# Optimization experiments

Measured on AMD Instinct MI355X. Metric: run time of the kernel, lower is better.

Reference implementation:

```python
import jax, jax.numpy as jnp
import numpy as np

WD, WH, WW = 6, 6, 6
NUM_HEADS = 8
EPS = 1e-5


def setup_inputs() -> dict:
    key = jax.random.key(0)
    ks = jax.random.split(key, 4)
    B, C, D, H, W = 1, 128, 48, 48, 48
    return {
        "q_map": jax.random.normal(ks[0], (B, C, D, H, W), dtype=jnp.float32),
        "k_map": jax.random.normal(ks[1], (B, C, D, H, W), dtype=jnp.float32),
        "v_map": jax.random.normal(ks[2], (B, C, D, H, W), dtype=jnp.float32),
        "gamma_q": jnp.ones((C,), jnp.float32),
        "beta_q": jnp.zeros((C,), jnp.float32),
        "gamma_kv": jnp.ones((C,), jnp.float32),
        "beta_kv": jnp.zeros((C,), jnp.float32),
        "proj_w": jax.random.normal(ks[3], (C, C), dtype=jnp.float32) * (1.0 / np.sqrt(C)),
        "proj_b": jnp.zeros((C,), jnp.float32),
    }


def _layernorm(x, g, b):
    m = jnp.mean(x, axis=-1, keepdims=True)
    v = jnp.mean(jnp.square(x - m), axis=-1, keepdims=True)
    return (x - m) * jax.lax.rsqrt(v + EPS) * g + b


def _window_partition(x):
    # x: (B, D, H, W, C) -> windows: (B*nD*nH*nW, wd*wh*ww, C)
    B, D, H, W, C = x.shape
    pd, ph, pw = (WD - D % WD) % WD, (WH - H % WH) % WH, (WW - W % WW) % WW
    if pd or ph or pw:
        x = jnp.pad(x, ((0, 0), (0, pd), (0, ph), (0, pw), (0, 0)))
    Dp, Hp, Wp = D + pd, H + ph, W + pw
    x = x.reshape(B, Dp // WD, WD, Hp // WH, WH, Wp // WW, WW, C)
    x = jnp.transpose(x, (0, 1, 3, 5, 2, 4, 6, 7))
    return x.reshape(-1, WD * WH * WW, C), (D, H, W, Dp, Hp, Wp)


def _window_reverse(windows, meta):
    D, H, W, Dp, Hp, Wp = meta
    C = windows.shape[-1]
    nD, nH, nW = Dp // WD, Hp // WH, Wp // WW
    B = windows.shape[0] // (nD * nH * nW)
    x = windows.reshape(B, nD, nH, nW, WD, WH, WW, C)
    x = jnp.transpose(x, (0, 1, 4, 2, 5, 3, 6, 7)).reshape(B, Dp, Hp, Wp, C)
    return x[:, :D, :H, :W, :]


def reference(q_map, k_map, v_map, gamma_q, beta_q, gamma_kv, beta_kv, proj_w, proj_b):
    # (B, C, D, H, W) -> (B, D, H, W, C)
    q_map = jnp.transpose(q_map, (0, 2, 3, 4, 1))
    k_map = jnp.transpose(k_map, (0, 2, 3, 4, 1))
    v_map = jnp.transpose(v_map, (0, 2, 3, 4, 1))

    q, meta = _window_partition(q_map)
    k, _ = _window_partition(k_map)
    v, _ = _window_partition(v_map)

    q = _layernorm(q, gamma_q, beta_q)
    k = _layernorm(k, gamma_kv, beta_kv)
    v = _layernorm(v, gamma_kv, beta_kv)

    Bw, Nq, C = q.shape
    dh = C // NUM_HEADS
    q = q.reshape(Bw, Nq, NUM_HEADS, dh)
    k = k.reshape(Bw, -1, NUM_HEADS, dh)
    v = v.reshape(Bw, -1, NUM_HEADS, dh)

    scale = 1.0 / np.sqrt(dh).astype(np.float32)
    scores = jnp.einsum("bqhd,bkhd->bhqk", q, k) * scale  # (Bw, h, Nq, Nk)
    attn = jax.nn.softmax(scores, axis=-1)
    out = jnp.einsum("bhqk,bkhd->bqhd", attn, v).reshape(Bw, Nq, C)

    out = out @ proj_w.T + proj_b
    out = _window_reverse(out, meta)
    return jnp.transpose(out, (0, 4, 1, 2, 3))  # (B, C, D, H, W)
```

## Files before the change

### kernel.cpp

```cpp
#include <hip/hip_runtime.h>
#include <hip/hip_bf16.h>

typedef short s16x8 __attribute__((ext_vector_type(8)));
typedef float f32x2 __attribute__((ext_vector_type(2)));
typedef float f32x4 __attribute__((ext_vector_type(4)));
typedef float f32x16 __attribute__((ext_vector_type(16)));
typedef unsigned int u32;
typedef unsigned short u16;
typedef u32 u32x4v __attribute__((ext_vector_type(4)));

#define TOK 216
#define T1 448
#define T2 896
#define SP 110592
#define BUF0 0
#define VOFF 57344
#define WOFF 122880
#define GBOFF 155648
#define LDS_OLD 157696
#define LDS_NEW 155648
#define TENB 28311552ull
#define WSNEED (3ull*TENB + 32768ull)
#define QSCALE 0.360673760f

__device__ __forceinline__ u32 pack2(float a, float b) {
  u16 lo = __builtin_bit_cast(u16, __float2bfloat16(a));
  u16 hi = __builtin_bit_cast(u16, __float2bfloat16(b));
  return (u32)lo | ((u32)hi << 16);
}
__device__ __forceinline__ int swz(int row, int inner) {
  return inner ^ ((row & 7) << 4);
}
__device__ __forceinline__ int swzk(int row, int inner) {
  return inner ^ ((row & 15) << 4);
}
__device__ __forceinline__ void gload16(const void* g, void* l) {
  __builtin_amdgcn_global_load_lds(
      (const __attribute__((address_space(1))) void*)g,
      (__attribute__((address_space(3))) void*)l, 16, 0, 0);
}

__device__ __forceinline__ void ln_stats(const f32x2* xv, float& mA, float& rA,
                                         float& mB, float& rB) {
  float sA = 0.f, s2A = 0.f, sB = 0.f, s2B = 0.f;
#pragma unroll
  for (int c = 0; c < 32; ++c) {
    sA += xv[c].x; s2A += xv[c].x * xv[c].x;
    sB += xv[c].y; s2B += xv[c].y * xv[c].y;
  }
  sA += __shfl_xor(sA, 1); s2A += __shfl_xor(s2A, 1);
  sB += __shfl_xor(sB, 1); s2B += __shfl_xor(s2B, 1);
  sA += __shfl_xor(sA, 2); s2A += __shfl_xor(s2A, 2);
  sB += __shfl_xor(sB, 2); s2B += __shfl_xor(s2B, 2);
  mA = sA * (1.0f / 128.0f);
  rA = rsqrtf(s2A * (1.0f / 128.0f) - mA * mA + 1e-5f);
  mB = sB * (1.0f / 128.0f);
  rB = rsqrtf(s2B * (1.0f / 128.0f) - mB * mB + 1e-5f);
}

template<bool MASK>
__device__ __forceinline__ void attn_stepN(const char* smem, int h, int kt,
                                           s16x8 qfh, int lane,
                                           f32x16& acc, float& lsum) {
  const int half = lane >> 5;
  const int krow = kt * 32 + (lane & 31);
  s16x8 kf = *(const s16x8*)(smem + BUF0 + krow * 256 +
                             swzk(krow, h * 32 + half * 16));
  f32x16 st = __builtin_amdgcn_mfma_f32_32x32x16_bf16(kf, qfh, (f32x16){}, 0, 0, 0);
  const int vrow = h * 16 + (lane & 15);
  s16x8 vf0 = *(const s16x8*)(smem + VOFF + vrow * 512 +
                              swz(vrow, kt * 64 + half * 16));
  s16x8 vf1 = *(const s16x8*)(smem + VOFF + vrow * 512 +
                              swz(vrow, kt * 64 + 32 + half * 16));
  const int NR = MASK ? 12 : 16;
  u32 A[8];
  float ts0 = 0.f, ts1 = 0.f;
#pragma unroll
  for (int i = 0; i < 8; ++i) {
    float p0 = (2 * i < NR) ? __builtin_amdgcn_exp2f(st[2 * i]) : 0.f;
    float p1 = (2 * i + 1 < NR) ? __builtin_amdgcn_exp2f(st[2 * i + 1]) : 0.f;
    if (i & 1) ts1 += p0 + p1; else ts0 += p0 + p1;
    A[i] = pack2(p0, p1);
  }
  lsum += ts0 + ts1;
  s16x8 pf0 = __builtin_bit_cast(s16x8, (u32x4v){A[0], A[1], A[2], A[3]});
  s16x8 pf1 = __builtin_bit_cast(s16x8, (u32x4v){A[4], A[5], A[6], A[7]});
  acc = __builtin_amdgcn_mfma_f32_32x32x16_bf16(vf0, pf0, acc, 0, 0, 0);
  acc = __builtin_amdgcn_mfma_f32_32x32x16_bf16(vf1, pf1, acc, 0, 0, 0);
}

template<bool MASK>
__device__ __forceinline__ void attn_stepF(const char* smem, int h, int kt,
                                           s16x8 qfh, int lane,
                                           f32x16& acc, float& lsum) {
  const int half = lane >> 5;
  const int krow = kt * 32 + (lane & 31);
  s16x8 kf = *(const s16x8*)(smem + BUF0 + krow * 256 +
                             swz(krow, h * 32 + half * 16));
  f32x16 st = __builtin_amdgcn_mfma_f32_32x32x16_bf16(kf, qfh, (f32x16){}, 0, 0, 0);
  const int vrow = h * 16 + (lane & 15);
  s16x8 vf0 = *(const s16x8*)(smem + VOFF + vrow * 512 +
                              swz(vrow, kt * 64 + half * 16));
  s16x8 vf1 = *(const s16x8*)(smem + VOFF + vrow * 512 +
                              swz(vrow, kt * 64 + 32 + half * 16));
  const int NR = MASK ? 12 : 16;
  u32 A[8];
  float ts0 = 0.f, ts1 = 0.f;
#pragma unroll
  for (int i = 0; i < 8; ++i) {
    float p0 = (2 * i < NR) ? __builtin_amdgcn_exp2f(st[2 * i]) : 0.f;
    float p1 = (2 * i + 1 < NR) ? __builtin_amdgcn_exp2f(st[2 * i + 1]) : 0.f;
    if (i & 1) ts1 += p0 + p1; else ts0 += p0 + p1;
    A[i] = pack2(p0, p1);
  }
  lsum += ts0 + ts1;
  s16x8 pf0 = __builtin_bit_cast(s16x8, (u32x4v){A[0], A[1], A[2], A[3]});
  s16x8 pf1 = __builtin_bit_cast(s16x8, (u32x4v){A[4], A[5], A[6], A[7]});
  acc = __builtin_amdgcn_mfma_f32_32x32x16_bf16(vf0, pf0, acc, 0, 0, 0);
  acc = __builtin_amdgcn_mfma_f32_32x32x16_bf16(vf1, pf1, acc, 0, 0, 0);
}

extern "C" __global__ __launch_bounds__(256)
void lnpre_kernel(const float* __restrict__ qm, const float* __restrict__ km,
                  const float* __restrict__ vm,
                  const float* __restrict__ gq, const float* __restrict__ bq,
                  const float* __restrict__ gkv, const float* __restrict__ bkv,
                  const float* __restrict__ pw,
                  u16* __restrict__ qn, u16* __restrict__ kn,
                  u16* __restrict__ vn, u16* __restrict__ wbf) {
  const int tid = threadIdx.x;
  const int bid = blockIdx.x;
  if (bid >= 2304) {
#pragma unroll
    for (int k = 0; k < 32; ++k) {
      int idx = tid + 256 * k;
      f32x2 w2 = *(const f32x2*)(pw + idx * 2);
      ((u32*)wbf)[idx] = pack2(w2.x, w2.y);
    }
    return;
  }
  __shared__ float lf[6144];
  __shared__ float gb[512];
  const int d = bid / 48, h = bid - d * 48;
  const int dh = d * 2304 + h * 48;
  if (tid < 128) {
    gb[tid] = gq[tid]; gb[128 + tid] = bq[tid];
    gb[256 + tid] = gkv[tid]; gb[384 + tid] = bkv[tid];
  }
  const int w = tid >> 2, q = tid & 3;
#pragma unroll 1
  for (int t = 0; t < 3; ++t) {
    const float* src = t == 0 ? qm : (t == 1 ? km : vm);
    u16* dst = t == 0 ? qn : (t == 1 ? kn : vn);
    const float* g = (t == 0) ? gb : gb + 256;
    const float* b = (t == 0) ? gb + 128 : gb + 384;
    const float scale = (t == 0) ? QSCALE : 1.0f;
#pragma unroll
    for (int k = 0; k < 6; ++k) {
      int j = tid + 256 * k;
      int ch = j / 12, wq = j - ch * 12;
      *(f32x4*)(lf + ch * 48 + wq * 4) =
          *(const f32x4*)(src + (long)ch * SP + dh + wq * 4);
    }
    __syncthreads();
    if (tid < 192) {
      float s = 0.f, s2 = 0.f;
#pragma unroll
      for (int c = 0; c < 32; ++c) {
        float x = lf[(q + 4 * c) * 48 + w];
        s += x; s2 += x * x;
      }
      s += __shfl_xor(s, 1); s2 += __shfl_xor(s2, 1);
      s += __shfl_xor(s, 2); s2 += __shfl_xor(s2, 2);
      float m = s * (1.f / 128.f);
      float r = rsqrtf(s2 * (1.f / 128.f) - m * m + 1e-5f);
      u32x4v* op = (u32x4v*)(dst + (long)(dh + w) * 128 + 32 * q);
#pragma unroll
      for (int v4 = 0; v4 < 4; ++v4) {
        u32x4v pk;
#pragma unroll
        for (int e = 0; e < 4; ++e) {
          int ch = 32 * q + v4 * 8 + 2 * e;
          float y0 = ((lf[ch * 48 + w] - m) * r * g[ch] + b[ch]) * scale;
          float y1 = ((lf[(ch + 1) * 48 + w] - m) * r * g[ch + 1] + b[ch + 1]) * scale;
          pk[e] = pack2(y0, y1);
        }
        op[v4] = pk;
      }
    }
    __syncthreads();
  }
}

extern "C" __global__ __launch_bounds__(T2, 1)
void attn2_kernel(const u16* __restrict__ qn, const u16* __restrict__ kn,
                  const u16* __restrict__ vn, const u16* __restrict__ wbf,
                  const float* __restrict__ pb, float* __restrict__ out) {
  extern __shared__ __align__(16) char smem[];
  const int tid = threadIdx.x;
  const int lane = tid & 63;
  const int wv = tid >> 6;
  const int wq = wv % 7;
  const int hb = (wv / 7) * 4;
  const int bid = blockIdx.x;
  const int wid = ((bid & 7) << 6) | (bid >> 3);
  const int wd = wid >> 6, wh = (wid >> 3) & 7, ww = wid & 7;
  const int wd6 = wd * 6, wh6 = wh * 6, ww6 = ww * 6;
  const int boff = wd6 * 2304 + wh6 * 48 + ww6;

  for (int uu = wv; uu < 140; uu += 14) {
    const u16* s; char* d;
    if (uu < 54) {
      int u = uu, row = 4 * u + (lane >> 4);
      int tq = row / 6;
      int g = (wd6 + tq / 6) * 2304 + (wh6 + tq % 6) * 48 + ww6 + row % 6;
      s = qn + g * 128 + (((lane & 15) ^ (row & 15)) << 3);
      d = smem + BUF0 + u * 1024;
    } else if (uu < 108) {
      int u = uu - 54, row = 4 * u + (lane >> 4);
      int tq = row / 6;
      int g = (wd6 + tq / 6) * 2304 + (wh6 + tq % 6) * 48 + ww6 + row % 6;
      s = vn + g * 128 + ((lane & 15) << 3);
      d = smem + VOFF + u * 1024;
    } else {
      int u = uu - 108, row = 4 * u + (lane >> 4);
      s = wbf + row * 128 + (((lane & 15) ^ (row & 15)) << 3);
      d = smem + WOFF + u * 1024;
    }
    gload16(s, d);
  }
  __syncthreads();

  s16x8 qf[4];
  {
    int row = wq * 32 + (lane & 31);
    int ib = (lane >> 5) * 16;
#pragma unroll
    for (int j = 0; j < 4; ++j)
      qf[j] = *(const s16x8*)(smem + BUF0 + row * 256 +
                              swzk(row, (hb + j) * 32 + ib));
  }
  __syncthreads();

  for (int uu = wv; uu < 54; uu += 14) {
    int row = 4 * uu + (lane >> 4);
    int tq = row / 6;
    int g = (wd6 + tq / 6) * 2304 + (wh6 + tq % 6) * 48 + ww6 + row % 6;
    gload16(kn + g * 128 + (((lane & 15) ^ (row & 15)) << 3),
            smem + BUF0 + uu * 1024);
  }
  u32 tr[16];
#pragma unroll
  for (int k = 0; k < 8; ++k) {
    int u = tid + 896 * k;
    if (u < 6912) {
      int t = (u >> 6) * 2, c2 = u & 63;
      tr[2 * k]     = *(const u32*)(smem + VOFF + t * 256 + c2 * 4);
      tr[2 * k + 1] = *(const u32*)(smem + VOFF + t * 256 + 256 + c2 * 4);
    }
  }
  __syncthreads();

#pragma unroll
  for (int k = 0; k < 8; ++k) {
    int u = tid + 896 * k;
    if (u < 6912) {
      int t = (u >> 6) * 2, c2 = u & 63;
      int st = (t & ~12) | ((t & 4) << 1) | ((t & 8) >> 1);
      int c = 2 * c2;
      u32 w0 = (tr[2 * k] & 0xFFFFu) | (tr[2 * k + 1] << 16);
      u32 w1 = (tr[2 * k] >> 16) | (tr[2 * k + 1] & 0xFFFF0000u);
      *(u32*)(smem + VOFF + c * 512 + ((st * 2) ^ ((c & 7) << 4))) = w0;
      *(u32*)(smem + VOFF + (c + 1) * 512 + ((st * 2) ^ (((c + 1) & 7) << 4))) = w1;
    }
  }
  if (tid < 128) {
    int x = (tid & 7) << 4;
    *(u32*)(smem + VOFF + tid * 512 + (424 ^ x)) = 0;
    *(u32*)(smem + VOFF + tid * 512 + (428 ^ x)) = 0;
    *(u32*)(smem + VOFF + tid * 512 + (440 ^ x)) = 0;
    *(u32*)(smem + VOFF + tid * 512 + (444 ^ x)) = 0;
  }
  __syncthreads();

  u32 oPk[4][4];
#pragma unroll
  for (int hp = 0; hp < 2; ++hp) {
    const int h0 = hb + 2 * hp, h1 = h0 + 1;
    f32x16 a0 = {}, a1 = {};
    float l0 = 0.f, l1 = 0.f;
#pragma unroll 2
    for (int kt = 0; kt < 6; ++kt) {
      attn_stepN<false>(smem, h0, kt, qf[2 * hp], lane, a0, l0);
      attn_stepN<false>(smem, h1, kt, qf[2 * hp + 1], lane, a1, l1);
    }
    attn_stepN<true>(smem, h0, 6, qf[2 * hp], lane, a0, l0);
    attn_stepN<true>(smem, h1, 6, qf[2 * hp + 1], lane, a1, l1);
    l0 += __shfl_xor(l0, 32);
    l1 += __shfl_xor(l1, 32);
    float i0 = 1.0f / l0, i1 = 1.0f / l1;
#pragma unroll
    for (int r = 0; r < 4; ++r) {
      oPk[2 * hp][r]     = pack2(a0[2 * r] * i0, a0[2 * r + 1] * i0);
      oPk[2 * hp + 1][r] = pack2(a1[2 * r] * i1, a1[2 * r + 1] * i1);
    }
  }
  __syncthreads();

  {
    const int tok = wq * 32 + (lane & 31);
    const int half = lane >> 5;
#pragma unroll
    for (int j = 0; j < 4; ++j) {
      int chb = (hb + j) * 32 + half * 8;
      *(u32*)(smem + BUF0 + tok * 256 + swzk(tok, chb))      = oPk[j][0];
      *(u32*)(smem + BUF0 + tok * 256 + swzk(tok, chb + 4))  = oPk[j][1];
      *(u32*)(smem + BUF0 + tok * 256 + swzk(tok, chb + 16)) = oPk[j][2];
      *(u32*)(smem + BUF0 + tok * 256 + swzk(tok, chb + 20)) = oPk[j][3];
    }
  }
  __syncthreads();

  {
    int tok = wv * 16 + (lane & 15);
    s16x8 bfr[4];
#pragma unroll
    for (int kk = 0; kk < 4; ++kk)
      bfr[kk] = *(const s16x8*)(smem + BUF0 + tok * 256 +
                                swzk(tok, kk * 64 + (lane >> 4) * 16));
    bool tokValid = tok < TOK;
    int tdd = tok / 36, trr = tok - tdd * 36;
    int thh = trr / 6, tww = trr - thh * 6;
    int pos = boff + tdd * 2304 + thh * 48 + tww;
#pragma unroll 1
    for (int jt = 0; jt < 8; ++jt) {
      f32x4 acc = {};
#pragma unroll
      for (int kk = 0; kk < 4; ++kk) {
        int rw = jt * 16 + (lane & 15);
        s16x8 af = *(const s16x8*)(smem + WOFF + rw * 256 +
                                   swzk(rw, kk * 64 + (lane >> 4) * 16));
        acc = __builtin_amdgcn_mfma_f32_16x16x32_bf16(af, bfr[kk], acc, 0, 0, 0);
      }
      f32x4 pbv = *(const f32x4*)(pb + jt * 16 + (lane >> 4) * 4);
      if (tokValid) {
#pragma unroll
        for (int r = 0; r < 4; ++r) {
          int j = jt * 16 + (lane >> 4) * 4 + r;
          out[j * SP + pos] = acc[r] + pbv[r];
        }
      }
    }
  }
}

extern "C" __global__ __launch_bounds__(T1, 2)
void ca3d_kernel(const float* __restrict__ qm, const float* __restrict__ km,
                 const float* __restrict__ vm,
                 const float* __restrict__ gq, const float* __restrict__ bq,
                 const float* __restrict__ gkv, const float* __restrict__ bkv,
                 const float* __restrict__ pw, const float* __restrict__ pb,
                 float* __restrict__ out) {
  extern __shared__ __align__(16) char smem[];
  const int tid = threadIdx.x;
  const int lane = tid & 63;
  const int wv = tid >> 6;
  const int bid = blockIdx.x;
  const int wid = ((bid & 7) << 6) | (bid >> 3);
  const int wd = wid >> 6, wh = (wid >> 3) & 7, ww = wid & 7;
  const int boff = wd * 6 * 2304 + wh * 6 * 48 + ww * 6;

  for (int i = tid * 16; i < VOFF + 65536; i += T1 * 16)
    *(f32x4*)(smem + i) = (f32x4){};
  if (tid < 128) {
    ((float*)(smem + GBOFF))[tid] = gq[tid];
    ((float*)(smem + GBOFF + 512))[tid] = bq[tid];
    ((float*)(smem + GBOFF + 1024))[tid] = gkv[tid];
    ((float*)(smem + GBOFF + 1536))[tid] = bkv[tid];
  }
  const bool lnAct = tid < 432;
  const int tp = tid >> 2;
  const int cbase = (tid & 3) * 32;
  const int tA = tp * 2, tB = tA + 1;
  int td = tA / 36, tr_ = tA - td * 36;
  int th_ = tr_ / 6, tw_ = tr_ - th_ * 6;
  const int gpos = boff + td * 2304 + th_ * 48 + tw_;
  const int vposA = (tA & ~0xC) | ((tA & 4) << 1) | ((tA & 8) >> 1);

  f32x2 qv[32], kv[32], vv[32];
  if (lnAct) {
#pragma unroll
    for (int c = 0; c < 32; ++c)
      qv[c] = *(const f32x2*)(qm + gpos + (cbase + c) * SP);
#pragma unroll
    for (int c = 0; c < 32; ++c)
      kv[c] = *(const f32x2*)(km + gpos + (cbase + c) * SP);
  }
  __syncthreads();
  const float* gql = (const float*)(smem + GBOFF);
  const float* bql = (const float*)(smem + GBOFF + 512);
  const float* gkl = (const float*)(smem + GBOFF + 1024);
  const float* bkl = (const float*)(smem + GBOFF + 1536);
  if (lnAct) {
    float mA, rA, mB, rB;
    ln_stats(qv, mA, rA, mB, rB);
#pragma unroll
    for (int c = 0; c < 32; c += 2) {
      int cc = cbase + c;
      float g0 = gql[cc], g1 = gql[cc + 1], b0 = bql[cc], b1 = bql[cc + 1];
      *(u32*)(smem + BUF0 + tA * 256 + swz(tA, cc * 2)) =
          pack2(((qv[c].x - mA) * rA * g0 + b0) * QSCALE,
                ((qv[c + 1].x - mA) * rA * g1 + b1) * QSCALE);
      *(u32*)(smem + BUF0 + tB * 256 + swz(tB, cc * 2)) =
          pack2(((qv[c].y - mB) * rB * g0 + b0) * QSCALE,
                ((qv[c + 1].y - mB) * rB * g1 + b1) * QSCALE);
    }
#pragma unroll
    for (int c = 0; c < 32; ++c)
      vv[c] = *(const f32x2*)(vm + gpos + (cbase + c) * SP);
  }
  __syncthreads();
  s16x8 qf[8];
  {
    int row = wv * 32 + (lane & 31);
    int ib = (lane >> 5) * 16;
#pragma unroll
    for (int h = 0; h < 8; ++h)
      qf[h] = *(const s16x8*)(smem + BUF0 + row * 256 + swz(row, h * 32 + ib));
  }
  __syncthreads();
  if (lnAct) {
    {
      float mA, rA, mB, rB;
      ln_stats(kv, mA, rA, mB, rB);
#pragma unroll
      for (int c = 0; c < 32; c += 2) {
        int cc = cbase + c;
        float g0 = gkl[cc], g1 = gkl[cc + 1], b0 = bkl[cc], b1 = bkl[cc + 1];
        *(u32*)(smem + BUF0 + tA * 256 + swz(tA, cc * 2)) =
            pack2((kv[c].x - mA) * rA * g0 + b0,
                  (kv[c + 1].x - mA) * rA * g1 + b1);
        *(u32*)(smem + BUF0 + tB * 256 + swz(tB, cc * 2)) =
            pack2((kv[c].y - mB) * rB * g0 + b0,
                  (kv[c + 1].y - mB) * rB * g1 + b1);
      }
    }
    {
      float mA, rA, mB, rB;
      ln_stats(vv, mA, rA, mB, rB);
#pragma unroll
      for (int c = 0; c < 32; ++c) {
        int cc = cbase + c;
        float g0 = gkl[cc], b0 = bkl[cc];
        *(u32*)(smem + VOFF + cc * 512 + swz(cc, vposA * 2)) =
            pack2((vv[c].x - mA) * rA * g0 + b0,
                  (vv[c].y - mB) * rB * g0 + b0);
      }
    }
  }
  for (int i = tid; i < 8192; i += T1) {
    int j = i >> 6, c2 = i & 63;
    f32x2 w2 = *(const f32x2*)(pw + j * 128 + c2 * 2);
    *(u32*)(smem + WOFF + j * 256 + swz(j, c2 * 4)) = pack2(w2.x, w2.y);
  }
  __syncthreads();
  u32 oPk[8][4];
#pragma unroll
  for (int hp = 0; hp < 4; ++hp) {
    const int h0 = hp * 2, h1 = h0 + 1;
    f32x16 a0 = {}, a1 = {};
    float l0 = 0.f, l1 = 0.f;
#pragma unroll 1
    for (int kt = 0; kt < 6; ++kt) {
      attn_stepF<false>(smem, h0, kt, qf[h0], lane, a0, l0);
      attn_stepF<false>(smem, h1, kt, qf[h1], lane, a1, l1);
    }
    attn_stepF<true>(smem, h0, 6, qf[h0], lane, a0, l0);
    attn_stepF<true>(smem, h1, 6, qf[h1], lane, a1, l1);
    l0 += __shfl_xor(l0, 32);
    l1 += __shfl_xor(l1, 32);
    float i0 = 1.0f / l0, i1 = 1.0f / l1;
#pragma unroll
    for (int r = 0; r < 4; ++r) {
      oPk[h0][r] = pack2(a0[2 * r] * i0, a0[2 * r + 1] * i0);
      oPk[h1][r] = pack2(a1[2 * r] * i1, a1[2 * r + 1] * i1);
    }
  }
  __syncthreads();
  {
    const int tok = wv * 32 + (lane & 31);
    const int half = lane >> 5;
#pragma unroll
    for (int h = 0; h < 8; ++h) {
      int chb = h * 32 + half * 8;
      *(u32*)(smem + BUF0 + tok * 256 + swz(tok, chb))      = oPk[h][0];
      *(u32*)(smem + BUF0 + tok * 256 + swz(tok, chb + 4))  = oPk[h][1];
      *(u32*)(smem + BUF0 + tok * 256 + swz(tok, chb + 16)) = oPk[h][2];
      *(u32*)(smem + BUF0 + tok * 256 + swz(tok, chb + 20)) = oPk[h][3];
    }
  }
  __syncthreads();
#pragma unroll 1
  for (int ti = 0; ti < 2; ++ti) {
    int tt = wv * 2 + ti;
    int tok = tt * 16 + (lane & 15);
    s16x8 bfr[4];
#pragma unroll
    for (int kk = 0; kk < 4; ++kk)
      bfr[kk] = *(const s16x8*)(smem + BUF0 + tok * 256 +
                                swz(tok, kk * 64 + (lane >> 4) * 16));
    bool tokValid = tok < TOK;
    int tdd = tok / 36, trr = tok - tdd * 36;
    int thh = trr / 6, tww = trr - thh * 6;
    int pos = boff + tdd * 2304 + thh * 48 + tww;
#pragma unroll 1
    for (int jt = 0; jt < 8; ++jt) {
      f32x4 acc = {};
#pragma unroll
      for (int kk = 0; kk < 4; ++kk) {
        int rw = jt * 16 + (lane & 15);
        s16x8 af = *(const s16x8*)(smem + WOFF + rw * 256 +
                                   swz(rw, kk * 64 + (lane >> 4) * 16));
        acc = __builtin_amdgcn_mfma_f32_16x16x32_bf16(af, bfr[kk], acc, 0, 0, 0);
      }
      f32x4 pbv = *(const f32x4*)(pb + jt * 16 + (lane >> 4) * 4);
      if (tokValid) {
#pragma unroll
        for (int r = 0; r < 4; ++r) {
          int j = jt * 16 + (lane >> 4) * 4 + r;
          out[j * SP + pos] = acc[r] + pbv[r];
        }
      }
    }
  }
}

extern "C" void kernel_launch(void* const* d_in, const int* in_sizes, int n_in,
                              void* d_out, int out_size, void* d_ws, size_t ws_size,
                              hipStream_t stream) {
  const float* qm  = (const float*)d_in[0];
  const float* km  = (const float*)d_in[1];
  const float* vm  = (const float*)d_in[2];
  const float* gq  = (const float*)d_in[3];
  const float* bq  = (const float*)d_in[4];
  const float* gkv = (const float*)d_in[5];
  const float* bkv = (const float*)d_in[6];
  const float* pw  = (const float*)d_in[7];
  const float* pb  = (const float*)d_in[8];
  if (ws_size >= WSNEED) {
    u16* qn  = (u16*)d_ws;
    u16* kn  = (u16*)((char*)d_ws + TENB);
    u16* vn  = (u16*)((char*)d_ws + 2 * TENB);
    u16* wbf = (u16*)((char*)d_ws + 3 * TENB);
    hipLaunchKernelGGL(lnpre_kernel, dim3(2305), dim3(256), 0, stream,
                       qm, km, vm, gq, bq, gkv, bkv, pw, qn, kn, vn, wbf);
    hipLaunchKernelGGL(attn2_kernel, dim3(512), dim3(T2), LDS_NEW, stream,
                       qn, kn, vn, wbf, pb, (float*)d_out);
  } else {
    hipLaunchKernelGGL(ca3d_kernel, dim3(512), dim3(T1), LDS_OLD, stream,
                       qm, km, vm, gq, bq, gkv, bkv, pw, pb, (float*)d_out);
  }
}
```

Before: 149.9 us.

## Split attention into per-head-group kernel and separate projection kernel

Replaces the single 896-thread attention+projection kernel, which used about 152KB of LDS and ran one block per CU, with two kernels. The first handles half the heads per block, uses 60KB of static LDS to allow several blocks per CU, and writes the attention output back into the q buffer in place. The second does the output projection over rows of 48 tokens so the stores to the output are coalesced. The cost is an extra launch and a bf16 round trip of the attention output through global memory.

```diff
diff --git a/kernel.cpp b/kernel.cpp
--- a/kernel.cpp
+++ b/kernel.cpp
@@ -11,14 +11,13 @@
 
 #define TOK 216
 #define T1 448
-#define T2 896
 #define SP 110592
 #define BUF0 0
 #define VOFF 57344
 #define WOFF 122880
 #define GBOFF 155648
 #define LDS_OLD 157696
-#define LDS_NEW 155648
+#define VHOFF 28672
 #define TENB 28311552ull
 #define WSNEED (3ull*TENB + 32768ull)
 #define QSCALE 0.360673760f
@@ -30,9 +29,6 @@
 }
 __device__ __forceinline__ int swz(int row, int inner) {
   return inner ^ ((row & 7) << 4);
-}
-__device__ __forceinline__ int swzk(int row, int inner) {
-  return inner ^ ((row & 15) << 4);
 }
 __device__ __forceinline__ void gload16(const void* g, void* l) {
   __builtin_amdgcn_global_load_lds(
@@ -59,19 +55,19 @@
 }
 
 template<bool MASK>
-__device__ __forceinline__ void attn_stepN(const char* smem, int h, int kt,
+__device__ __forceinline__ void attn_stepH(const char* smem, int jloc, int kt,
                                            s16x8 qfh, int lane,
                                            f32x16& acc, float& lsum) {
   const int half = lane >> 5;
   const int krow = kt * 32 + (lane & 31);
-  s16x8 kf = *(const s16x8*)(smem + BUF0 + krow * 256 +
-                             swzk(krow, h * 32 + half * 16));
+  s16x8 kf = *(const s16x8*)(smem + krow * 128 +
+                             ((jloc * 32 + half * 16) ^ ((krow & 7) << 4)));
   f32x16 st = __builtin_amdgcn_mfma_f32_32x32x16_bf16(kf, qfh, (f32x16){}, 0, 0, 0);
-  const int vrow = h * 16 + (lane & 15);
-  s16x8 vf0 = *(const s16x8*)(smem + VOFF + vrow * 512 +
-                              swz(vrow, kt * 64 + half * 16));
-  s16x8 vf1 = *(const s16x8*)(smem + VOFF + vrow * 512 +
-                              swz(vrow, kt * 64 + 32 + half * 16));
+  const int vrow = jloc * 16 + (lane & 15);
+  s16x8 vf0 = *(const s16x8*)(smem + VHOFF + vrow * 512 +
+                              ((kt * 64 + half * 16) ^ ((vrow & 7) << 4)));
+  s16x8 vf1 = *(const s16x8*)(smem + VHOFF + vrow * 512 +
+                              ((kt * 64 + 32 + half * 16) ^ ((vrow & 7) << 4)));
   const int NR = MASK ? 12 : 16;
   u32 A[8];
   float ts0 = 0.f, ts1 = 0.f;
@@ -192,163 +188,167 @@
   }
 }
 
-extern "C" __global__ __launch_bounds__(T2, 1)
-void attn2_kernel(const u16* __restrict__ qn, const u16* __restrict__ kn,
-                  const u16* __restrict__ vn, const u16* __restrict__ wbf,
-                  const float* __restrict__ pb, float* __restrict__ out) {
-  extern __shared__ __align__(16) char smem[];
-  const int tid = threadIdx.x;
-  const int lane = tid & 63;
-  const int wv = tid >> 6;
-  const int wq = wv % 7;
-  const int hb = (wv / 7) * 4;
+extern "C" __global__ __launch_bounds__(448, 4)
+void attnh_kernel(u16* __restrict__ qn, const u16* __restrict__ kn,
+                  const u16* __restrict__ vn) {
+  __shared__ __align__(16) char smem[61440];
+  const int tid = threadIdx.x, lane = tid & 63, wv = tid >> 6;
+  const int half = lane >> 5;
   const int bid = blockIdx.x;
-  const int wid = ((bid & 7) << 6) | (bid >> 3);
-  const int wd = wid >> 6, wh = (wid >> 3) & 7, ww = wid & 7;
-  const int wd6 = wd * 6, wh6 = wh * 6, ww6 = ww * 6;
-  const int boff = wd6 * 2304 + wh6 * 48 + ww6;
-
-  for (int uu = wv; uu < 140; uu += 14) {
-    const u16* s; char* d;
-    if (uu < 54) {
-      int u = uu, row = 4 * u + (lane >> 4);
-      int tq = row / 6;
-      int g = (wd6 + tq / 6) * 2304 + (wh6 + tq % 6) * 48 + ww6 + row % 6;
-      s = qn + g * 128 + (((lane & 15) ^ (row & 15)) << 3);
-      d = smem + BUF0 + u * 1024;
-    } else if (uu < 108) {
-      int u = uu - 54, row = 4 * u + (lane >> 4);
-      int tq = row / 6;
-      int g = (wd6 + tq / 6) * 2304 + (wh6 + tq % 6) * 48 + ww6 + row % 6;
-      s = vn + g * 128 + ((lane & 15) << 3);
-      d = smem + VOFF + u * 1024;
-    } else {
-      int u = uu - 108, row = 4 * u + (lane >> 4);
-      s = wbf + row * 128 + (((lane & 15) ^ (row & 15)) << 3);
-      d = smem + WOFF + u * 1024;
-    }
-    gload16(s, d);
-  }
-  __syncthreads();
-
-  s16x8 qf[4];
-  {
-    int row = wq * 32 + (lane & 31);
-    int ib = (lane >> 5) * 16;
-#pragma unroll
-    for (int j = 0; j < 4; ++j)
-      qf[j] = *(const s16x8*)(smem + BUF0 + row * 256 +
-                              swzk(row, (hb + j) * 32 + ib));
-  }
-  __syncthreads();
-
-  for (int uu = wv; uu < 54; uu += 14) {
-    int row = 4 * uu + (lane >> 4);
+  const int wid = bid >> 1, hg = bid & 1;
+  const int wd6 = (wid >> 6) * 6, wh6 = ((wid >> 3) & 7) * 6, ww6 = (wid & 7) * 6;
+
+  for (int uu = wv; uu < 27; uu += 7) {
+    int row = 8 * uu + (lane >> 3);
     int tq = row / 6;
     int g = (wd6 + tq / 6) * 2304 + (wh6 + tq % 6) * 48 + ww6 + row % 6;
-    gload16(kn + g * 128 + (((lane & 15) ^ (row & 15)) << 3),
-            smem + BUF0 + uu * 1024);
-  }
+    gload16(kn + g * 128 + hg * 64 + (((lane & 7) ^ (row & 7)) << 3),
+            smem + uu * 1024);
+  }
+  for (int uu = wv; uu < 27; uu += 7) {
+    int row = 8 * uu + (lane >> 3);
+    int tq = row / 6;
+    int g = (wd6 + tq / 6) * 2304 + (wh6 + tq % 6) * 48 + ww6 + row % 6;
+    gload16(vn + g * 128 + hg * 64 + ((lane & 7) << 3),
+            smem + VHOFF + uu * 1024);
+  }
+  int qrow = wv * 32 + (lane & 31);
+  if (qrow > 215) qrow = 215;
+  int qtq = qrow / 6;
+  int qg = (wd6 + qtq / 6) * 2304 + (wh6 + qtq % 6) * 48 + ww6 + qrow % 6;
+  s16x8 qf[4];
+#pragma unroll
+  for (int j = 0; j < 4; ++j)
+    qf[j] = *(const s16x8*)(qn + qg * 128 + (hg * 4 + j) * 16 + half * 8);
+  __syncthreads();
+
   u32 tr[16];
 #pragma unroll
   for (int k = 0; k < 8; ++k) {
-    int u = tid + 896 * k;
-    if (u < 6912) {
-      int t = (u >> 6) * 2, c2 = u & 63;
-      tr[2 * k]     = *(const u32*)(smem + VOFF + t * 256 + c2 * 4);
-      tr[2 * k + 1] = *(const u32*)(smem + VOFF + t * 256 + 256 + c2 * 4);
-    }
-  }
-  __syncthreads();
-
+    int u = tid + 448 * k;
+    if (u < 3456) {
+      int t = (u >> 5) * 2, c2 = u & 31;
+      tr[2 * k]     = *(const u32*)(smem + VHOFF + t * 128 + c2 * 4);
+      tr[2 * k + 1] = *(const u32*)(smem + VHOFF + t * 128 + 128 + c2 * 4);
+    }
+  }
+  __syncthreads();
 #pragma unroll
   for (int k = 0; k < 8; ++k) {
-    int u = tid + 896 * k;
-    if (u < 6912) {
-      int t = (u >> 6) * 2, c2 = u & 63;
+    int u = tid + 448 * k;
+    if (u < 3456) {
+      int t = (u >> 5) * 2, c2 = u & 31;
       int st = (t & ~12) | ((t & 4) << 1) | ((t & 8) >> 1);
       int c = 2 * c2;
       u32 w0 = (tr[2 * k] & 0xFFFFu) | (tr[2 * k + 1] << 16);
       u32 w1 = (tr[2 * k] >> 16) | (tr[2 * k + 1] & 0xFFFF0000u);
-      *(u32*)(smem + VOFF + c * 512 + ((st * 2) ^ ((c & 7) << 4))) = w0;
-      *(u32*)(smem + VOFF + (c + 1) * 512 + ((st * 2) ^ (((c + 1) & 7) << 4))) = w1;
-    }
-  }
-  if (tid < 128) {
+      *(u32*)(smem + VHOFF + c * 512 + ((st * 2) ^ ((c & 7) << 4))) = w0;
+      *(u32*)(smem + VHOFF + (c + 1) * 512 + ((st * 2) ^ (((c + 1) & 7) << 4))) = w1;
+    }
+  }
+  if (tid < 64) {
     int x = (tid & 7) << 4;
-    *(u32*)(smem + VOFF + tid * 512 + (424 ^ x)) = 0;
-    *(u32*)(smem + VOFF + tid * 512 + (428 ^ x)) = 0;
-    *(u32*)(smem + VOFF + tid * 512 + (440 ^ x)) = 0;
-    *(u32*)(smem + VOFF + tid * 512 + (444 ^ x)) = 0;
+    *(u32*)(smem + VHOFF + tid * 512 + (424 ^ x)) = 0;
+    *(u32*)(smem + VHOFF + tid * 512 + (428 ^ x)) = 0;
+    *(u32*)(smem + VHOFF + tid * 512 + (440 ^ x)) = 0;
+    *(u32*)(smem + VHOFF + tid * 512 + (444 ^ x)) = 0;
   }
   __syncthreads();
 
   u32 oPk[4][4];
 #pragma unroll
   for (int hp = 0; hp < 2; ++hp) {
-    const int h0 = hb + 2 * hp, h1 = h0 + 1;
+    const int j0 = 2 * hp, j1 = j0 + 1;
     f32x16 a0 = {}, a1 = {};
     float l0 = 0.f, l1 = 0.f;
 #pragma unroll 2
     for (int kt = 0; kt < 6; ++kt) {
-      attn_stepN<false>(smem, h0, kt, qf[2 * hp], lane, a0, l0);
-      attn_stepN<false>(smem, h1, kt, qf[2 * hp + 1], lane, a1, l1);
-    }
-    attn_stepN<true>(smem, h0, 6, qf[2 * hp], lane, a0, l0);
-    attn_stepN<true>(smem, h1, 6, qf[2 * hp + 1], lane, a1, l1);
+      attn_stepH<false>(smem, j0, kt, qf[j0], lane, a0, l0);
+      attn_stepH<false>(smem, j1, kt, qf[j1], lane, a1, l1);
+    }
+    attn_stepH<true>(smem, j0, 6, qf[j0], lane, a0, l0);
+    attn_stepH<true>(smem, j1, 6, qf[j1], lane, a1, l1);
     l0 += __shfl_xor(l0, 32);
     l1 += __shfl_xor(l1, 32);
     float i0 = 1.0f / l0, i1 = 1.0f / l1;
 #pragma unroll
     for (int r = 0; r < 4; ++r) {
-      oPk[2 * hp][r]     = pack2(a0[2 * r] * i0, a0[2 * r + 1] * i0);
-      oPk[2 * hp + 1][r] = pack2(a1[2 * r] * i1, a1[2 * r + 1] * i1);
+      oPk[j0][r] = pack2(a0[2 * r] * i0, a0[2 * r + 1] * i0);
+      oPk[j1][r] = pack2(a1[2 * r] * i1, a1[2 * r + 1] * i1);
     }
   }
   __syncthreads();
 
   {
-    const int tok = wq * 32 + (lane & 31);
-    const int half = lane >> 5;
+    const int tok = wv * 32 + (lane & 31);
 #pragma unroll
     for (int j = 0; j < 4; ++j) {
-      int chb = (hb + j) * 32 + half * 8;
-      *(u32*)(smem + BUF0 + tok * 256 + swzk(tok, chb))      = oPk[j][0];
-      *(u32*)(smem + BUF0 + tok * 256 + swzk(tok, chb + 4))  = oPk[j][1];
-      *(u32*)(smem + BUF0 + tok * 256 + swzk(tok, chb + 16)) = oPk[j][2];
-      *(u32*)(smem + BUF0 + tok * 256 + swzk(tok, chb + 20)) = oPk[j][3];
-    }
-  }
-  __syncthreads();
-
-  {
-    int tok = wv * 16 + (lane & 15);
-    s16x8 bfr[4];
+      int chb = j * 32 + half * 8;
+      *(u32*)(smem + tok * 128 + ((chb)      ^ ((tok & 7) << 4))) = oPk[j][0];
+      *(u32*)(smem + tok * 128 + ((chb + 4)  ^ ((tok & 7) << 4))) = oPk[j][1];
+      *(u32*)(smem + tok * 128 + ((chb + 16) ^ ((tok & 7) << 4))) = oPk[j][2];
+      *(u32*)(smem + tok * 128 + ((chb + 20) ^ ((tok & 7) << 4))) = oPk[j][3];
+    }
+  }
+  __syncthreads();
+
+#pragma unroll
+  for (int it = 0; it < 4; ++it) {
+    int i = tid + 448 * it;
+    int row = i >> 3;
+    if (row < 216) {
+      int chunk = i & 7;
+      f32x4 v = *(const f32x4*)(smem + row * 128 +
+                                ((chunk * 16) ^ ((row & 7) << 4)));
+      int tq = row / 6;
+      int g = (wd6 + tq / 6) * 2304 + (wh6 + tq % 6) * 48 + ww6 + row % 6;
+      *(f32x4*)(qn + g * 128 + hg * 64 + chunk * 8) = v;
+    }
+  }
+}
+
+extern "C" __global__ __launch_bounds__(256, 3)
+void proj_kernel(const u16* __restrict__ on, const u16* __restrict__ wbf,
+                 const float* __restrict__ pb, float* __restrict__ out) {
+  __shared__ __align__(16) char smem[45056];
+  const int tid = threadIdx.x, lane = tid & 63, wv = tid >> 6;
+  const int bid = blockIdx.x;
+  const int dh = (bid / 48) * 2304 + (bid % 48) * 48;
+  for (int uu = wv; uu < 32; uu += 4) {
+    int row = 4 * uu + (lane >> 4);
+    gload16(wbf + row * 128 + (((lane & 15) ^ (row & 15)) << 3),
+            smem + uu * 1024);
+  }
+  for (int uu = wv; uu < 12; uu += 4) {
+    int row = 4 * uu + (lane >> 4);
+    gload16(on + (long)(dh + row) * 128 + (((lane & 15) ^ (row & 15)) << 3),
+            smem + 32768 + uu * 1024);
+  }
+  __syncthreads();
+#pragma unroll
+  for (int jj = 0; jj < 2; ++jj) {
+    int jt = wv * 2 + jj;
+    int rw = jt * 16 + (lane & 15);
+    s16x8 af[4];
 #pragma unroll
     for (int kk = 0; kk < 4; ++kk)
-      bfr[kk] = *(const s16x8*)(smem + BUF0 + tok * 256 +
-                                swzk(tok, kk * 64 + (lane >> 4) * 16));
-    bool tokValid = tok < TOK;
-    int tdd = tok / 36, trr = tok - tdd * 36;
-    int thh = trr / 6, tww = trr - thh * 6;
-    int pos = boff + tdd * 2304 + thh * 48 + tww;
-#pragma unroll 1
-    for (int jt = 0; jt < 8; ++jt) {
+      af[kk] = *(const s16x8*)(smem + rw * 256 +
+                               ((kk * 64 + (lane >> 4) * 16) ^ ((rw & 15) << 4)));
+    f32x4 pbv = *(const f32x4*)(pb + jt * 16 + (lane >> 4) * 4);
+#pragma unroll
+    for (int t = 0; t < 3; ++t) {
+      int tok = t * 16 + (lane & 15);
       f32x4 acc = {};
 #pragma unroll
       for (int kk = 0; kk < 4; ++kk) {
-        int rw = jt * 16 + (lane & 15);
-        s16x8 af = *(const s16x8*)(smem + WOFF + rw * 256 +
-                                   swzk(rw, kk * 64 + (lane >> 4) * 16));
-        acc = __builtin_amdgcn_mfma_f32_16x16x32_bf16(af, bfr[kk], acc, 0, 0, 0);
-      }
-      f32x4 pbv = *(const f32x4*)(pb + jt * 16 + (lane >> 4) * 4);
-      if (tokValid) {
-#pragma unroll
-        for (int r = 0; r < 4; ++r) {
-          int j = jt * 16 + (lane >> 4) * 4 + r;
-          out[j * SP + pos] = acc[r] + pbv[r];
-        }
+        s16x8 bfr = *(const s16x8*)(smem + 32768 + tok * 256 +
+                                    ((kk * 64 + (lane >> 4) * 16) ^ ((tok & 15) << 4)));
+        acc = __builtin_amdgcn_mfma_f32_16x16x32_bf16(af[kk], bfr, acc, 0, 0, 0);
+      }
+#pragma unroll
+      for (int r = 0; r < 4; ++r) {
+        int j = jt * 16 + (lane >> 4) * 4 + r;
+        out[(long)j * SP + dh + tok] = acc[r] + pbv[r];
       }
     }
   }
@@ -554,8 +554,10 @@
     u16* wbf = (u16*)((char*)d_ws + 3 * TENB);
     hipLaunchKernelGGL(lnpre_kernel, dim3(2305), dim3(256), 0, stream,
                        qm, km, vm, gq, bq, gkv, bkv, pw, qn, kn, vn, wbf);
-    hipLaunchKernelGGL(attn2_kernel, dim3(512), dim3(T2), LDS_NEW, stream,
-                       qn, kn, vn, wbf, pb, (float*)d_out);
+    hipLaunchKernelGGL(attnh_kernel, dim3(1024), dim3(448), 0, stream,
+                       qn, kn, vn);
+    hipLaunchKernelGGL(proj_kernel, dim3(2304), dim3(256), 0, stream,
+                       qn, wbf, pb, (float*)d_out);
   } else {
     hipLaunchKernelGGL(ca3d_kernel, dim3(512), dim3(T1), LDS_OLD, stream,
                        qm, km, vm, gq, bq, gkv, bkv, pw, pb, (float*)d_out);
```

Measured after the change: 139.6 us. 6.9% less time.
